# Kernel tuning notes

Measured on AMD Instinct MI355X. Metric: run time of the kernel, lower is better.

Reference implementation:

```python
import jax, jax.numpy as jnp
import numpy as np

B, NB, L, K, C, H = 4, 256, 64, 65, 512, 8
HD = C // H
SCALE = HD ** -0.5


def setup_inputs() -> dict:
    key = jax.random.key(0)
    k = jax.random.split(key, 6)
    x = jax.random.normal(k[0], (B, NB * L, C), dtype=jnp.float32)
    mask = jax.random.bernoulli(k[1], 0.3, (NB, L, K))
    d = jnp.arange(L)
    mask = mask.at[:, d, d].set(True)      # self edges always on
    mask = mask.at[:, :, L].set(True)      # block-node column always on
    edge_feats = jax.random.normal(k[2], (NB, L, K, 4), dtype=jnp.float32)
    qkv_w = jax.random.normal(k[3], (C, 3 * C), dtype=jnp.float32) * (C ** -0.5)
    qkv_b = jnp.zeros((3 * C,), dtype=jnp.float32)
    proj_w = jax.random.normal(k[4], (C, C), dtype=jnp.float32) * (C ** -0.5)
    proj_b = jnp.zeros((C,), dtype=jnp.float32)
    return {"x": x, "attn_mask": mask, "edge_feats": edge_feats,
            "qkv_w": qkv_w, "qkv_b": qkv_b, "proj_w": proj_w, "proj_b": proj_b}


def reference(x, attn_mask, edge_feats, qkv_w, qkv_b, proj_w, proj_b):
    # x: (B, N, C) with N = NB*L (no padding needed); pool = 1, layout LxL+1
    x_blk = x.reshape(B, NB, L, C)                       # query tokens per leaf block
    block_node = x_blk.mean(axis=2, keepdims=True)       # (B, NB, 1, C)
    kv = jnp.concatenate([x_blk, block_node], axis=2)    # (B, NB, K, C), K = L+1

    qkv_q = x_blk @ qkv_w + qkv_b
    qkv_kv = kv @ qkv_w + qkv_b
    q = qkv_q[..., :C].reshape(B, NB, L, H, HD)
    k = qkv_kv[..., C:2 * C].reshape(B, NB, K, H, HD)
    v = qkv_kv[..., 2 * C:].reshape(B, NB, K, H, HD)

    scores = jnp.einsum('bnqhd,bnkhd->bnqkh', q, k) * SCALE  # (B,NB,L,K,H)

    # physics bias: edge_feats[..., :4] broadcast over batch; special/diagonal overrides
    bp = jnp.broadcast_to(edge_feats[None, ..., :4], (B, NB, L, K, 4))
    bp = bp.at[:, :, :, L, :].set(0.0)
    bp = bp.at[:, :, :, L, 3].set(1.0)                    # block-node key column
    d = jnp.arange(L)
    bp = bp.at[:, :, d, d, :].set(0.0)
    bp = bp.at[:, :, d, d, 3].set(1.0)                    # self edge
    scores = scores + bp[..., 3:4]                        # channel 3 additive bias (all heads)

    mask = attn_mask[None, :, :, :, None]                 # (1,NB,L,K,1)
    scores = jnp.where(mask, scores, jnp.float32(-1e9))
    attn = jax.nn.softmax(scores, axis=3)

    out = jnp.einsum('bnqkh,bnkhd->bnqhd', attn, v).reshape(B, NB * L, C)
    return out @ proj_w + proj_b
```

## Files before the change

### kernel.cpp

```cpp
#include <hip/hip_runtime.h>
#include <hip/hip_bf16.h>
#include <math.h>

typedef unsigned short u16;
typedef __attribute__((ext_vector_type(8))) short s16x8;
typedef __attribute__((ext_vector_type(4))) float f32x4;

#define NB_ 256
#define L_  64
#define KK_ 65
#define C_  512
#define H_  8
#define NEDGE (256*64*65)
#define MTOT  65536

__device__ __forceinline__ float b2f(u16 u){
  union { unsigned int i; float f; } x; x.i = ((unsigned int)u) << 16; return x.f;
}
__device__ __forceinline__ u16 f2b(float f){
  union { float f; unsigned int i; } x; x.f = f;
  return (u16)((x.i + 0x7FFFu + ((x.i >> 16) & 1u)) >> 16);
}

__device__ __forceinline__ void gload_lds16(const u16* g, u16* l){
  __builtin_amdgcn_global_load_lds(
      (const __attribute__((address_space(1))) unsigned int*)g,
      (__attribute__((address_space(3))) unsigned int*)l,
      16, 0, 0);
}

__global__ void detect_dtype_kernel(const u16* __restrict__ x, int* __restrict__ flagdt){
  __shared__ int cnt;
  if (threadIdx.x == 0) cnt = 0;
  __syncthreads();
  u16 v = x[(size_t)threadIdx.x * 2 * 1001];
  int e = (v >> 7) & 0xFF;
  if (e >= 141) atomicAdd(&cnt, 1);
  __syncthreads();
  if (threadIdx.x == 0) *flagdt = (cnt >= 8) ? 1 : 0;
}

__global__ void detect_mask_kernel(const unsigned char* __restrict__ m, int* __restrict__ flag){
  __shared__ int ok1, ok2, ok4;
  if (threadIdx.x == 0){ ok1 = 1; ok2 = 1; ok4 = 1; }
  __syncthreads();
  size_t e = (size_t)threadIdx.x * 65 + 64;
  if (((const unsigned char*)m)[e] == 0)  atomicAnd(&ok1, 0);
  if (((const unsigned short*)m)[e] == 0) atomicAnd(&ok2, 0);
  if (((const unsigned int*)m)[e] == 0u)  atomicAnd(&ok4, 0);
  __syncthreads();
  if (threadIdx.x == 0){
    int f = 4;
    if (ok2) f = 2;
    if (ok1) f = 1;
    *flag = f;
  }
}

__global__ void convert_kernel(const void* __restrict__ src, u16* __restrict__ dst,
                               long n, const int* __restrict__ flagdt){
  long i = ((long)blockIdx.x * 256 + threadIdx.x) * 8;
  if (i >= n) return;
  if (*flagdt){
    const float* s = (const float*)src + i;
    u16 o[8];
    #pragma unroll
    for (int j = 0; j < 8; ++j) o[j] = f2b(s[j]);
    *(s16x8*)(dst + i) = *(const s16x8*)o;
  } else {
    *(s16x8*)(dst + i) = *(const s16x8*)((const u16*)src + i);
  }
}

__global__ void extract_edge_kernel(const void* __restrict__ src, u16* __restrict__ dst,
                                    const int* __restrict__ flagdt){
  long i = (long)blockIdx.x * 256 + threadIdx.x;
  if (i >= NEDGE) return;
  if (*flagdt) dst[i] = f2b(((const float*)src)[i*4 + 3]);
  else         dst[i] = ((const u16*)src)[i*4 + 3];
}

__global__ void transpose_conv_kernel(const void* __restrict__ in, u16* __restrict__ out,
                                      int R, int Cc, const int* __restrict__ flagdt){
  long i = (long)blockIdx.x * 256 + threadIdx.x;
  if (i < (long)R * Cc){
    int r = (int)(i / Cc), c = (int)(i % Cc);
    u16 v = (*flagdt) ? f2b(((const float*)in)[i]) : ((const u16*)in)[i];
    out[(long)c * R + r] = v;
  }
}

__global__ __launch_bounds__(256) void block_mean_kernel(const u16* __restrict__ x, u16* __restrict__ bm){
  int blk = blockIdx.x;
  const u16* xp = x + (long)blk * 64 * 512;
  for (int c = threadIdx.x; c < 512; c += 256){
    float s = 0.f;
    #pragma unroll
    for (int l = 0; l < 64; ++l) s += b2f(xp[l*512 + c]);
    bm[(long)blk * 512 + c] = f2b(s * 0.015625f);
  }
}

__global__ __launch_bounds__(256) void gemm_bt_kernel(
    const u16* __restrict__ A, const u16* __restrict__ BT,
    const u16* __restrict__ bias, u16* __restrict__ Cmat,
    int lda, int ldc, int Kdim, const int* __restrict__ flagdt, int out_mode,
    long row_off)
{
  __shared__ __align__(16) u16 As[128*32];
  __shared__ __align__(16) u16 Bs[128*32];
  const int t = threadIdx.x;
  const int lane = t & 63;
  const int w = t >> 6;
  const int wm = w & 1, wn = w >> 1;
  const int quad = lane >> 4;
  const int ml = lane & 15;
  const long colbase = (long)blockIdx.x * 128;
  const long rowbase = (long)blockIdx.y * 128;
  const int of = out_mode ? *flagdt : 0;

  const f32x4 zero4 = {0.f, 0.f, 0.f, 0.f};
  f32x4 acc[4][4];
  #pragma unroll
  for (int i = 0; i < 4; ++i)
    #pragma unroll
    for (int j = 0; j < 4; ++j) acc[i][j] = zero4;

  const int c0 = t,       r0 = c0 >> 2, s0 = c0 & 3, g0 = s0 ^ ((r0 >> 1) & 3);
  const int c1 = t + 256, r1 = c1 >> 2, s1 = c1 & 3, g1 = s1 ^ ((r1 >> 1) & 3);
  const u16* Arow0 = A + (rowbase + r0) * (long)lda + g0*8;
  const u16* Arow1 = A + (rowbase + r1) * (long)lda + g1*8;
  const u16* Brow0 = BT + (colbase + r0) * (long)Kdim + g0*8;
  const u16* Brow1 = BT + (colbase + r1) * (long)Kdim + g1*8;

  u16* AsW0 = As + w*512;
  u16* AsW1 = As + 2048 + w*512;
  u16* BsW0 = Bs + w*512;
  u16* BsW1 = Bs + 2048 + w*512;

  for (int k0 = 0; k0 < Kdim; k0 += 32){
    __syncthreads();
    gload_lds16(Arow0 + k0, AsW0);
    gload_lds16(Arow1 + k0, AsW1);
    gload_lds16(Brow0 + k0, BsW0);
    gload_lds16(Brow1 + k0, BsW1);
    __syncthreads();
    s16x8 af[4], bfr[4];
    #pragma unroll
    for (int i = 0; i < 4; ++i){
      int m = wm*64 + i*16 + ml;
      af[i]  = *(const s16x8*)(As + m*32 + ((quad ^ ((m>>1)&3)))*8);
      int n = wn*64 + i*16 + ml;
      bfr[i] = *(const s16x8*)(Bs + n*32 + ((quad ^ ((n>>1)&3)))*8);
    }
    #pragma unroll
    for (int i = 0; i < 4; ++i)
      #pragma unroll
      for (int j = 0; j < 4; ++j)
        acc[i][j] = __builtin_amdgcn_mfma_f32_16x16x32_bf16(af[i], bfr[j], acc[i][j], 0, 0, 0);
  }

  #pragma unroll
  for (int j = 0; j < 4; ++j){
    long col = colbase + wn*64 + j*16 + ml;
    float bv = b2f(bias[col]);
    #pragma unroll
    for (int i = 0; i < 4; ++i){
      long row = row_off + rowbase + wm*64 + i*16 + quad*4;
      if (of){
        float* Cf = (float*)Cmat;
        #pragma unroll
        for (int r = 0; r < 4; ++r)
          Cf[(row + r) * (long)ldc + col] = acc[i][j][r] + bv;
      } else {
        #pragma unroll
        for (int r = 0; r < 4; ++r)
          Cmat[(row + r) * (long)ldc + col] = f2b(acc[i][j][r] + bv);
      }
    }
  }
}

__global__ __launch_bounds__(256) void attn_kernel(
    const u16* __restrict__ Y, const u16* __restrict__ kvb,
    const u16* __restrict__ edgeb, const unsigned char* __restrict__ mask,
    const int* __restrict__ flagp, u16* __restrict__ AO, int blk0)
{
  __shared__ __align__(16) u16 q_s [64*72];
  __shared__ __align__(16) u16 k_s [80*72];
  __shared__ __align__(16) u16 vT_s[64*104];
  __shared__ __align__(16) u16 P_s [64*104];

  const int t = threadIdx.x;
  const int lane = t & 63;
  const int w = t >> 6;
  const int quad = lane >> 4;
  const int ml = lane & 15;
  const int lblk = blockIdx.x;
  const int blk = blk0 + lblk;
  const int h = blockIdx.y;
  const int nb = blk & (NB_ - 1);
  const long yrow0 = (long)lblk * 64;
  const int flag = *flagp;

  for (int i = t; i < 64*31; i += 256){ int d = i/31, c = 65 + (i%31); vT_s[d*104 + c] = 0; }
  for (int i = t; i < 64*16; i += 256){ int l = i>>4,  c = 80 + (i&15); P_s[l*104 + c] = 0; }
  for (int i = t; i < 15*72; i += 256){ k_s[65*72 + i] = 0; }

  for (int c = t; c < 512; c += 256){
    int l = c >> 3, c8 = c & 7;
    *(s16x8*)(q_s + l*72 + c8*8) = *(const s16x8*)(Y + (yrow0 + l)*1536 + h*64 + c8*8);
  }
  for (int c = t; c < 520; c += 256){
    int kk = c >> 3, c8 = c & 7;
    const u16 *srck, *srcv;
    if (kk < 64){
      const u16* base = Y + (yrow0 + kk)*1536;
      srck = base + 512  + h*64 + c8*8;
      srcv = base + 1024 + h*64 + c8*8;
    } else {
      const u16* base = kvb + (long)blk * 1024;
      srck = base + h*64 + c8*8;
      srcv = base + 512 + h*64 + c8*8;
    }
    *(s16x8*)(k_s + kk*72 + c8*8) = *(const s16x8*)srck;
    s16x8 vv = *(const s16x8*)srcv;
    #pragma unroll
    for (int j = 0; j < 8; ++j) vT_s[(c8*8 + j)*104 + kk] = (u16)vv[j];
  }
  __syncthreads();

  const f32x4 zero4 = {0.f, 0.f, 0.f, 0.f};
  f32x4 sacc[5];
  #pragma unroll
  for (int j = 0; j < 5; ++j) sacc[j] = zero4;
  #pragma unroll
  for (int s = 0; s < 2; ++s){
    s16x8 aq = *(const s16x8*)(q_s + (w*16 + ml)*72 + s*32 + quad*8);
    #pragma unroll
    for (int j = 0; j < 5; ++j){
      s16x8 bk = *(const s16x8*)(k_s + (j*16 + ml)*72 + s*32 + quad*8);
      sacc[j] = __builtin_amdgcn_mfma_f32_16x16x32_bf16(aq, bk, sacc[j], 0, 0, 0);
    }
  }

  float sv[5][4];
  #pragma unroll
  for (int j = 0; j < 5; ++j){
    int kk = j*16 + ml;
    #pragma unroll
    for (int r = 0; r < 4; ++r){
      int l = w*16 + quad*4 + r;
      float xv = -1e9f;
      if (kk < 65){
        long e = ((long)nb*64 + l)*65 + kk;
        bool mt;
        if (flag == 1)      mt = mask[e] != 0;
        else if (flag == 2) mt = ((const unsigned short*)mask)[e] != 0;
        else                mt = ((const unsigned int*)mask)[e]   != 0u;
        if (mt){
          float bias = (kk == 64 || kk == l) ? 1.0f : b2f(edgeb[e]);
          xv = sacc[j][r]*0.125f + bias;
        }
      }
      sv[j][r] = xv;
    }
  }
  #pragma unroll
  for (int r = 0; r < 4; ++r){
    float mx = sv[0][r];
    #pragma unroll
    for (int j = 1; j < 5; ++j) mx = fmaxf(mx, sv[j][r]);
    #pragma unroll
    for (int o = 1; o < 16; o <<= 1) mx = fmaxf(mx, __shfl_xor(mx, o, 64));
    float sm = 0.f;
    #pragma unroll
    for (int j = 0; j < 5; ++j){ float e = __expf(sv[j][r] - mx); sv[j][r] = e; sm += e; }
    #pragma unroll
    for (int o = 1; o < 16; o <<= 1) sm += __shfl_xor(sm, o, 64);
    float inv = 1.0f / sm;
    #pragma unroll
    for (int j = 0; j < 5; ++j) sv[j][r] *= inv;
  }
  #pragma unroll
  for (int j = 0; j < 5; ++j){
    int kk = j*16 + ml;
    #pragma unroll
    for (int r = 0; r < 4; ++r)
      P_s[(w*16 + quad*4 + r)*104 + kk] = f2b(sv[j][r]);
  }
  __syncthreads();

  f32x4 oacc[4];
  #pragma unroll
  for (int j = 0; j < 4; ++j) oacc[j] = zero4;
  #pragma unroll
  for (int s = 0; s < 3; ++s){
    s16x8 ap = *(const s16x8*)(P_s + (w*16 + ml)*104 + s*32 + quad*8);
    #pragma unroll
    for (int j = 0; j < 4; ++j){
      s16x8 bv = *(const s16x8*)(vT_s + (j*16 + ml)*104 + s*32 + quad*8);
      oacc[j] = __builtin_amdgcn_mfma_f32_16x16x32_bf16(ap, bv, oacc[j], 0, 0, 0);
    }
  }
  #pragma unroll
  for (int j = 0; j < 4; ++j){
    int d = j*16 + ml;
    #pragma unroll
    for (int r = 0; r < 4; ++r){
      int l = w*16 + quad*4 + r;
      AO[(yrow0 + l)*512 + h*64 + d] = f2b(oacc[j][r]);
    }
  }
}

extern "C" void kernel_launch(void* const* d_in, const int* in_sizes, int n_in,
                              void* d_out, int out_size, void* d_ws, size_t ws_size,
                              hipStream_t stream)
{
  const void* x_raw     = d_in[0];
  const unsigned char* mask = (const unsigned char*)d_in[1];
  const void* edge_raw  = d_in[2];
  const void* qkvw_raw  = d_in[3];
  const void* qkvb_raw  = d_in[4];
  const void* projw_raw = d_in[5];
  const void* projb_raw = d_in[6];

  char* ws = (char*)d_ws;
  size_t off = 0;
  int*  flagm  = (int*)ws;
  int*  flagdt = (int*)(ws + 4);         off += 1024;
  u16*  XC  = (u16*)(ws + off);          off += (size_t)33554432*2;
  u16*  EB  = (u16*)(ws + off);          off += (size_t)NEDGE*2;
  u16*  WT  = (u16*)(ws + off);          off += (size_t)1536*512*2;
  u16*  PT  = (u16*)(ws + off);          off += (size_t)512*512*2;
  u16*  QB  = (u16*)(ws + off);          off += 4096;
  u16*  PB  = (u16*)(ws + off);          off += 4096;
  u16*  BM  = (u16*)(ws + off);          off += (size_t)1024*512*2;
  u16*  KVB = (u16*)(ws + off);          off += (size_t)1024*1024*2;
  u16*  Y   = (u16*)(ws + off);          off += (size_t)MTOT*1536*2;
  u16*  AO  = (u16*)(ws + off);          off += (size_t)MTOT*512*2;

  detect_dtype_kernel<<<dim3(1), dim3(128), 0, stream>>>((const u16*)x_raw, flagdt);
  detect_mask_kernel<<<dim3(1), dim3(128), 0, stream>>>(mask, flagm);

  convert_kernel<<<dim3(33554432/8/256), dim3(256), 0, stream>>>(x_raw, XC, 33554432, flagdt);
  extract_edge_kernel<<<dim3((NEDGE + 255)/256), dim3(256), 0, stream>>>(edge_raw, EB, flagdt);
  transpose_conv_kernel<<<dim3((512*1536 + 255)/256), dim3(256), 0, stream>>>(qkvw_raw, WT, 512, 1536, flagdt);
  transpose_conv_kernel<<<dim3((512*512  + 255)/256), dim3(256), 0, stream>>>(projw_raw, PT, 512, 512, flagdt);
  convert_kernel<<<dim3(1), dim3(256), 0, stream>>>(qkvb_raw, QB, 1536, flagdt);
  convert_kernel<<<dim3(1), dim3(256), 0, stream>>>(projb_raw, PB, 512, flagdt);

  block_mean_kernel<<<dim3(1024), dim3(256), 0, stream>>>(XC, BM);
  gemm_bt_kernel<<<dim3(8, 8), dim3(256), 0, stream>>>(BM, WT + 512*512, QB + 512, KVB, 512, 1024, 512, flagdt, 0, 0);

  gemm_bt_kernel<<<dim3(12, MTOT/128), dim3(256), 0, stream>>>(XC, WT, QB, Y, 512, 1536, 512, flagdt, 0, 0);
  attn_kernel<<<dim3(1024, 8), dim3(256), 0, stream>>>(Y, KVB, EB, mask, flagm, AO, 0);
  gemm_bt_kernel<<<dim3(4, MTOT/128), dim3(256), 0, stream>>>(AO, PT, PB, (u16*)d_out, 512, 512, 512, flagdt, 1, 0);
}
```

Baseline: 686.2 us.

## Precompute masked bias, remap workgroups for XCD locality, load Q straight to registers

Mask, diagonal and block-node overrides are folded into a single precomputed bf16 bias tensor, so the attention kernel reads one value per score instead of the mask plus the edge bias. GEMM and attention workgroup IDs are remapped so neighbouring tiles (and all heads of one block) land on the same XCD, which should improve L2 reuse. Q fragments are now loaded directly from global memory into registers, dropping the q shared-memory stage, and the vT transpose store is rotated to reduce LDS bank conflicts. Attention launch bounds request 4 waves per SIMD. The bias tensor is built on every call, and the remap assumes the grid size is a multiple of 8.

```diff
diff --git a/kernel.cpp b/kernel.cpp
--- a/kernel.cpp
+++ b/kernel.cpp
@@ -72,12 +72,26 @@
   }
 }
 
-__global__ void extract_edge_kernel(const void* __restrict__ src, u16* __restrict__ dst,
-                                    const int* __restrict__ flagdt){
+__global__ void build_bias_kernel(const void* __restrict__ edge,
+                                  const unsigned char* __restrict__ mask,
+                                  const int* __restrict__ flagdt,
+                                  const int* __restrict__ flagm,
+                                  u16* __restrict__ dst){
   long i = (long)blockIdx.x * 256 + threadIdx.x;
   if (i >= NEDGE) return;
-  if (*flagdt) dst[i] = f2b(((const float*)src)[i*4 + 3]);
-  else         dst[i] = ((const u16*)src)[i*4 + 3];
+  int kk = (int)(i % 65);
+  long rowi = i / 65;
+  int l = (int)(rowi & 63);
+  int fm = *flagm;
+  bool mt;
+  if (fm == 1)      mt = mask[i] != 0;
+  else if (fm == 2) mt = ((const unsigned short*)mask)[i] != 0;
+  else              mt = ((const unsigned int*)mask)[i]   != 0u;
+  float v;
+  if (!mt)                      v = -1e9f;
+  else if (kk == 64 || kk == l) v = 1.0f;
+  else v = (*flagdt) ? ((const float*)edge)[i*4 + 3] : b2f(((const u16*)edge)[i*4 + 3]);
+  dst[i] = f2b(v);
 }
 
 __global__ void transpose_conv_kernel(const void* __restrict__ in, u16* __restrict__ out,
@@ -115,8 +129,15 @@
   const int wm = w & 1, wn = w >> 1;
   const int quad = lane >> 4;
   const int ml = lane & 15;
-  const long colbase = (long)blockIdx.x * 128;
-  const long rowbase = (long)blockIdx.y * 128;
+
+  const int nwg  = gridDim.x * gridDim.y;
+  const int orig = blockIdx.y * gridDim.x + blockIdx.x;
+  int lid = orig;
+  if ((nwg & 7) == 0) lid = (orig & 7) * (nwg >> 3) + (orig >> 3);
+  const int bx = lid % gridDim.x;
+  const int by = lid / gridDim.x;
+  const long colbase = (long)bx * 128;
+  const long rowbase = (long)by * 128;
   const int of = out_mode ? *flagdt : 0;
 
   const f32x4 zero4 = {0.f, 0.f, 0.f, 0.f};
@@ -181,12 +202,10 @@
   }
 }
 
-__global__ __launch_bounds__(256) void attn_kernel(
+__global__ __launch_bounds__(256, 4) void attn_kernel(
     const u16* __restrict__ Y, const u16* __restrict__ kvb,
-    const u16* __restrict__ edgeb, const unsigned char* __restrict__ mask,
-    const int* __restrict__ flagp, u16* __restrict__ AO, int blk0)
+    const u16* __restrict__ biasb, u16* __restrict__ AO)
 {
-  __shared__ __align__(16) u16 q_s [64*72];
   __shared__ __align__(16) u16 k_s [80*72];
   __shared__ __align__(16) u16 vT_s[64*104];
   __shared__ __align__(16) u16 P_s [64*104];
@@ -196,21 +215,22 @@
   const int w = t >> 6;
   const int quad = lane >> 4;
   const int ml = lane & 15;
-  const int lblk = blockIdx.x;
-  const int blk = blk0 + lblk;
-  const int h = blockIdx.y;
+
+  const int orig = blockIdx.y * gridDim.x + blockIdx.x;
+  const int lid  = (orig & 7) * 1024 + (orig >> 3);
+  const int blk  = lid >> 3;
+  const int h    = lid & 7;
   const int nb = blk & (NB_ - 1);
-  const long yrow0 = (long)lblk * 64;
-  const int flag = *flagp;
+  const long yrow0 = (long)blk * 64;
+
+  const u16* qrow = Y + (yrow0 + w*16 + ml)*1536 + h*64 + quad*8;
+  s16x8 aq0 = *(const s16x8*)(qrow);
+  s16x8 aq1 = *(const s16x8*)(qrow + 32);
 
   for (int i = t; i < 64*31; i += 256){ int d = i/31, c = 65 + (i%31); vT_s[d*104 + c] = 0; }
   for (int i = t; i < 64*16; i += 256){ int l = i>>4,  c = 80 + (i&15); P_s[l*104 + c] = 0; }
   for (int i = t; i < 15*72; i += 256){ k_s[65*72 + i] = 0; }
 
-  for (int c = t; c < 512; c += 256){
-    int l = c >> 3, c8 = c & 7;
-    *(s16x8*)(q_s + l*72 + c8*8) = *(const s16x8*)(Y + (yrow0 + l)*1536 + h*64 + c8*8);
-  }
   for (int c = t; c < 520; c += 256){
     int kk = c >> 3, c8 = c & 7;
     const u16 *srck, *srcv;
@@ -226,7 +246,10 @@
     *(s16x8*)(k_s + kk*72 + c8*8) = *(const s16x8*)srck;
     s16x8 vv = *(const s16x8*)srcv;
     #pragma unroll
-    for (int j = 0; j < 8; ++j) vT_s[(c8*8 + j)*104 + kk] = (u16)vv[j];
+    for (int j = 0; j < 8; ++j){
+      int jj = (j + c8) & 7;
+      vT_s[(c8*8 + jj)*104 + kk] = (u16)vv[jj];
+    }
   }
   __syncthreads();
 
@@ -235,13 +258,11 @@
   #pragma unroll
   for (int j = 0; j < 5; ++j) sacc[j] = zero4;
   #pragma unroll
-  for (int s = 0; s < 2; ++s){
-    s16x8 aq = *(const s16x8*)(q_s + (w*16 + ml)*72 + s*32 + quad*8);
-    #pragma unroll
-    for (int j = 0; j < 5; ++j){
-      s16x8 bk = *(const s16x8*)(k_s + (j*16 + ml)*72 + s*32 + quad*8);
-      sacc[j] = __builtin_amdgcn_mfma_f32_16x16x32_bf16(aq, bk, sacc[j], 0, 0, 0);
-    }
+  for (int j = 0; j < 5; ++j){
+    s16x8 bk0 = *(const s16x8*)(k_s + (j*16 + ml)*72 + quad*8);
+    sacc[j] = __builtin_amdgcn_mfma_f32_16x16x32_bf16(aq0, bk0, sacc[j], 0, 0, 0);
+    s16x8 bk1 = *(const s16x8*)(k_s + (j*16 + ml)*72 + 32 + quad*8);
+    sacc[j] = __builtin_amdgcn_mfma_f32_16x16x32_bf16(aq1, bk1, sacc[j], 0, 0, 0);
   }
 
   float sv[5][4];
@@ -254,14 +275,7 @@
       float xv = -1e9f;
       if (kk < 65){
         long e = ((long)nb*64 + l)*65 + kk;
-        bool mt;
-        if (flag == 1)      mt = mask[e] != 0;
-        else if (flag == 2) mt = ((const unsigned short*)mask)[e] != 0;
-        else                mt = ((const unsigned int*)mask)[e]   != 0u;
-        if (mt){
-          float bias = (kk == 64 || kk == l) ? 1.0f : b2f(edgeb[e]);
-          xv = sacc[j][r]*0.125f + bias;
-        }
+        xv = sacc[j][r]*0.125f + b2f(biasb[e]);
       }
       sv[j][r] = xv;
     }
@@ -345,7 +359,7 @@
   detect_mask_kernel<<<dim3(1), dim3(128), 0, stream>>>(mask, flagm);
 
   convert_kernel<<<dim3(33554432/8/256), dim3(256), 0, stream>>>(x_raw, XC, 33554432, flagdt);
-  extract_edge_kernel<<<dim3((NEDGE + 255)/256), dim3(256), 0, stream>>>(edge_raw, EB, flagdt);
+  build_bias_kernel<<<dim3((NEDGE + 255)/256), dim3(256), 0, stream>>>(edge_raw, mask, flagdt, flagm, EB);
   transpose_conv_kernel<<<dim3((512*1536 + 255)/256), dim3(256), 0, stream>>>(qkvw_raw, WT, 512, 1536, flagdt);
   transpose_conv_kernel<<<dim3((512*512  + 255)/256), dim3(256), 0, stream>>>(projw_raw, PT, 512, 512, flagdt);
   convert_kernel<<<dim3(1), dim3(256), 0, stream>>>(qkvb_raw, QB, 1536, flagdt);
@@ -355,6 +369,6 @@
   gemm_bt_kernel<<<dim3(8, 8), dim3(256), 0, stream>>>(BM, WT + 512*512, QB + 512, KVB, 512, 1024, 512, flagdt, 0, 0);
 
   gemm_bt_kernel<<<dim3(12, MTOT/128), dim3(256), 0, stream>>>(XC, WT, QB, Y, 512, 1536, 512, flagdt, 0, 0);
-  attn_kernel<<<dim3(1024, 8), dim3(256), 0, stream>>>(Y, KVB, EB, mask, flagm, AO, 0);
+  attn_kernel<<<dim3(1024, 8), dim3(256), 0, stream>>>(Y, KVB, EB, AO);
   gemm_bt_kernel<<<dim3(4, MTOT/128), dim3(256), 0, stream>>>(AO, PT, PB, (u16*)d_out, 512, 512, 512, flagdt, 1, 0);
 }
```

Result: faster. 601.0 us (-12.4%).
